# Performance work log

Hardware: AMD Instinct MI355X
Metric: run time of the kernel (lower is better)

## Reference

```python
import jax, jax.numpy as jnp
import numpy as np

# Matches init_kwargs: zip(dilation_rates, sequence_lengths)
DILATION_RATES = (1, 2, 4)
SEQUENCE_LENGTHS = (2048, 4096, 8192)


def setup_inputs() -> dict:
    key = jax.random.key(0)
    qkv = jax.random.normal(key, (4, 8192, 3, 16, 64), dtype=jnp.float32)
    return {"qkv": qkv}


def _attend(x, scale):
    # x: (B', Nseg, 3, h, d) -- vanilla softmax attention over axis Nseg
    q, k, v = x[:, :, 0], x[:, :, 1], x[:, :, 2]
    scores = jnp.einsum('bnhd,bmhd->bhnm', q, k) * scale
    attn = jax.nn.softmax(scores, axis=-1)
    return jnp.einsum('bhnm,bmhd->bnhd', attn, v)  # (B', Nseg, h, d)


def reference(qkv):
    b, n, _, h, d = qkv.shape
    scale = 1.0 / jnp.sqrt(jnp.asarray(d, qkv.dtype))  # softmax_scale=None default
    out = jnp.zeros((b, n, h, d), qkv.dtype)
    for r, s in zip(DILATION_RATES, SEQUENCE_LENGTHS):
        nseg = n // s
        # 'b (n s) qkv h d -> b n s qkv h d' then dilated slice [::r]
        x = qkv.reshape(b, nseg, s, 3, h, d)[:, :, ::r]  # (b, nseg, sp, 3, h, d)
        sp = x.shape[2]
        # 'b n s qkv h d -> (b s) n qkv h d'
        x = x.transpose(0, 2, 1, 3, 4, 5).reshape(b * sp, nseg, 3, h, d)
        o = _attend(x, scale)  # (b*sp, nseg, h, d)
        # '(b s) n h d -> b n s h d'
        o = o.reshape(b, sp, nseg, h, d).transpose(0, 2, 1, 3, 4)
        # strided scatter-add back into the full-length accumulator
        out = out.reshape(b, nseg, s, h, d).at[:, :, ::r].add(o).reshape(b, n, h, d)
    # final global normalization over the sequence dim (as in the source)
    return out / out.sum(axis=1, keepdims=True)
```

## Files before the change

kernel.cpp:

```cpp
#include <hip/hip_runtime.h>

constexpr int   Bn    = 4;
constexpr int   Nn    = 8192;
constexpr int   Hn    = 16;
constexpr int   Dn    = 64;
constexpr int   ROW   = 3 * Hn * Dn;
constexpr long long QKV_B = (long long)Nn * ROW;
constexpr int   OUT_N = Hn * Dn;
constexpr long long OUT_B = (long long)Nn * OUT_N;
constexpr long long OUT_TOT = (long long)Bn * OUT_B;
constexpr int   NBLK  = 2048;
constexpr int   BLKS_PER_B = 512;

using v4f = __attribute__((ext_vector_type(4))) float;
using v4u = __attribute__((ext_vector_type(4))) unsigned int;

template<int CTRL>
__device__ __forceinline__ float dpp_add(float x) {
  int mv = __builtin_amdgcn_update_dpp(0, __float_as_int(x), CTRL, 0xF, 0xF, true);
  return x + __int_as_float(mv);
}
__device__ __forceinline__ float row16_sum(float x) {
  x = dpp_add<0xB1>(x);
  x = dpp_add<0x4E>(x);
  x = dpp_add<0x124>(x);
  x = dpp_add<0x128>(x);
  return x;
}

__device__ __forceinline__ unsigned short f2bf_rne(float x) {
  unsigned u = __float_as_uint(x);
  u += 0x7FFFu + ((u >> 16) & 1u);
  return (unsigned short)(u >> 16);
}

struct Frag {
  float q[4][4], k[4][4], v[4][4];
};

__device__ __forceinline__ void load_frag(Frag& f, const float* __restrict__ qb,
                                          int j) {
#pragma unroll
  for (int m = 0; m < 4; ++m) {
    const float* rp = qb + (size_t)(m * 2048 + j) * ROW;
    float4 t;
    t = *(const float4*)(rp);
    f.q[m][0] = t.x; f.q[m][1] = t.y; f.q[m][2] = t.z; f.q[m][3] = t.w;
    t = *(const float4*)(rp + 1024);
    f.k[m][0] = t.x; f.k[m][1] = t.y; f.k[m][2] = t.z; f.k[m][3] = t.w;
    t = *(const float4*)(rp + 2048);
    f.v[m][0] = t.x; f.v[m][1] = t.y; f.v[m][2] = t.z; f.v[m][3] = t.w;
  }
}

template<bool USE_BF16>
__device__ __forceinline__ void compute_frag(const Frag& f, int j, size_t obase,
                                             float* __restrict__ out,
                                             unsigned short* __restrict__ ws16,
                                             float* cs) {
  float S[4][4];
#pragma unroll
  for (int m = 0; m < 4; ++m)
#pragma unroll
    for (int m2 = 0; m2 < 4; ++m2) {
      float s = f.q[m][0] * f.k[m2][0] + f.q[m][1] * f.k[m2][1] +
                f.q[m][2] * f.k[m2][2] + f.q[m][3] * f.k[m2][3];
      S[m][m2] = row16_sum(s) * 0.125f;
    }

  float acc[4][4];

#pragma unroll
  for (int m = 0; m < 4; ++m) {
    float mx = fmaxf(fmaxf(S[m][0], S[m][1]), fmaxf(S[m][2], S[m][3]));
    float e0 = __expf(S[m][0] - mx);
    float e1 = __expf(S[m][1] - mx);
    float e2 = __expf(S[m][2] - mx);
    float e3 = __expf(S[m][3] - mx);
    float inv = 1.0f / (e0 + e1 + e2 + e3);
    e0 *= inv; e1 *= inv; e2 *= inv; e3 *= inv;
#pragma unroll
    for (int c = 0; c < 4; ++c)
      acc[m][c] = e0 * f.v[0][c] + e1 * f.v[1][c] +
                  e2 * f.v[2][c] + e3 * f.v[3][c];
  }

  if ((j & 1) == 0) {
#pragma unroll
    for (int m = 0; m < 4; ++m) {
      const int a  = m & 1;
      const int b2 = a + 2;
      float sa = S[m][a], sb = S[m][b2];
      float mx = fmaxf(sa, sb);
      float ea = __expf(sa - mx);
      float eb = __expf(sb - mx);
      float inv = 1.0f / (ea + eb);
      ea *= inv; eb *= inv;
#pragma unroll
      for (int c = 0; c < 4; ++c)
        acc[m][c] += ea * f.v[a][c] + eb * f.v[b2][c];
    }
  }

  if ((j & 3) == 0) {
#pragma unroll
    for (int m = 0; m < 4; ++m)
#pragma unroll
      for (int c = 0; c < 4; ++c)
        acc[m][c] += f.v[m][c];
  }

#pragma unroll
  for (int m = 0; m < 4; ++m) {
    const size_t oi = obase + (size_t)(m * 2048 + j) * OUT_N;
    if (USE_BF16) {
      ushort4 st;
      st.x = f2bf_rne(acc[m][0]); st.y = f2bf_rne(acc[m][1]);
      st.z = f2bf_rne(acc[m][2]); st.w = f2bf_rne(acc[m][3]);
      *(ushort4*)(ws16 + oi) = st;
    } else {
      *(float4*)(out + oi) =
          make_float4(acc[m][0], acc[m][1], acc[m][2], acc[m][3]);
    }
    cs[0] += acc[m][0]; cs[1] += acc[m][1];
    cs[2] += acc[m][2]; cs[3] += acc[m][3];
  }
}

template<bool USE_BF16>
__global__ __launch_bounds__(256) void dil_main(const float* __restrict__ qkv,
                                                float* __restrict__ out,
                                                unsigned short* __restrict__ ws16,
                                                float* __restrict__ partial) {
  const int tid  = threadIdx.x;
  const int bid  = blockIdx.x;
  const int b    = bid >> 9;
  const int j0   = (bid & 511) * 4;

  const float* qb = qkv + (size_t)b * QKV_B + tid * 4;
  const size_t obase = (size_t)b * OUT_B + tid * 4;

  float cs[4] = {0.f, 0.f, 0.f, 0.f};

  Frag A, B;
  load_frag(A, qb, j0);
  load_frag(B, qb, j0 + 1);
  __builtin_amdgcn_sched_barrier(0);
  compute_frag<USE_BF16>(A, j0, obase, out, ws16, cs);
  load_frag(A, qb, j0 + 2);
  __builtin_amdgcn_sched_barrier(0);
  compute_frag<USE_BF16>(B, j0 + 1, obase, out, ws16, cs);
  load_frag(B, qb, j0 + 3);
  __builtin_amdgcn_sched_barrier(0);
  compute_frag<USE_BF16>(A, j0 + 2, obase, out, ws16, cs);
  compute_frag<USE_BF16>(B, j0 + 3, obase, out, ws16, cs);

  *(float4*)(partial + (size_t)bid * 1024 + tid * 4) =
      make_float4(cs[0], cs[1], cs[2], cs[3]);
}

__global__ __launch_bounds__(256) void dil_recip(const float* __restrict__ partial,
                                                 float* __restrict__ recip) {
  const int i = blockIdx.x * 256 + threadIdx.x;
  const int b = i >> 10;
  const int w = i & 1023;
  const float* p = partial + (size_t)b * BLKS_PER_B * 1024 + w;
  double s0 = 0.0, s1 = 0.0, s2 = 0.0, s3 = 0.0;
  double s4 = 0.0, s5 = 0.0, s6 = 0.0, s7 = 0.0;
  for (int r = 0; r < BLKS_PER_B; r += 8) {
    float f0 = p[(size_t)(r + 0) * 1024];
    float f1 = p[(size_t)(r + 1) * 1024];
    float f2 = p[(size_t)(r + 2) * 1024];
    float f3 = p[(size_t)(r + 3) * 1024];
    float f4 = p[(size_t)(r + 4) * 1024];
    float f5 = p[(size_t)(r + 5) * 1024];
    float f6 = p[(size_t)(r + 6) * 1024];
    float f7 = p[(size_t)(r + 7) * 1024];
    s0 += (double)f0; s1 += (double)f1; s2 += (double)f2; s3 += (double)f3;
    s4 += (double)f4; s5 += (double)f5; s6 += (double)f6; s7 += (double)f7;
  }
  double s = ((s0 + s1) + (s2 + s3)) + ((s4 + s5) + (s6 + s7));
  recip[i] = (float)(1.0 / s);
}

__global__ __launch_bounds__(256) void dil_scale_bf16(const unsigned short* __restrict__ ws16,
                                                      float* __restrict__ out,
                                                      const float* __restrict__ recip) {
  const long long u = (long long)blockIdx.x * 256 + threadIdx.x;
  const long long e = u * 8;
  const int b  = (int)(e >> 23);
  const int h  = (int)((e >> 6) & 15);
  const int q8 = (int)((e >> 3) & 7);

  const float4 r0 = ((const float4*)recip)[((b * 16 + h) << 4) + q8 * 2];
  const float4 r1 = ((const float4*)recip)[((b * 16 + h) << 4) + q8 * 2 + 1];

  const uint4 raw = *(const uint4*)(ws16 + e);
  v4f o0, o1;
  o0[0] = __uint_as_float((raw.x & 0xFFFFu) << 16) * r0.x;
  o0[1] = __uint_as_float((raw.x & 0xFFFF0000u))   * r0.y;
  o0[2] = __uint_as_float((raw.y & 0xFFFFu) << 16) * r0.z;
  o0[3] = __uint_as_float((raw.y & 0xFFFF0000u))   * r0.w;
  o1[0] = __uint_as_float((raw.z & 0xFFFFu) << 16) * r1.x;
  o1[1] = __uint_as_float((raw.z & 0xFFFF0000u))   * r1.y;
  o1[2] = __uint_as_float((raw.w & 0xFFFFu) << 16) * r1.z;
  o1[3] = __uint_as_float((raw.w & 0xFFFF0000u))   * r1.w;
  __builtin_nontemporal_store(o0, (v4f*)(out + e));
  __builtin_nontemporal_store(o1, (v4f*)(out + e + 4));
}

__global__ __launch_bounds__(256) void dil_scale_f32(float* __restrict__ out,
                                                     const float* __restrict__ recip) {
  const long long f = (long long)blockIdx.x * 256 + threadIdx.x;
  const int d4 = (int)(f & 15);
  const int h  = (int)((f >> 4) & 15);
  const int b  = (int)(f >> 21);
  const float4 r = ((const float4*)recip)[(b * 16 + h) * 16 + d4];
  float4 o = ((const float4*)out)[f];
  o.x *= r.x; o.y *= r.y; o.z *= r.z; o.w *= r.w;
  ((float4*)out)[f] = o;
}

extern "C" void kernel_launch(void* const* d_in, const int* in_sizes, int n_in,
                              void* d_out, int out_size, void* d_ws, size_t ws_size,
                              hipStream_t stream) {
  const float* qkv = (const float*)d_in[0];
  float* out = (float*)d_out;

  const size_t bf16_bytes    = (size_t)OUT_TOT * 2;
  const size_t partial_bytes = (size_t)NBLK * 1024 * 4;
  const size_t recip_bytes   = 4096 * sizeof(float);

  bool use_bf16 = (bf16_bytes + partial_bytes + recip_bytes) <= ws_size;

  unsigned short* ws16 = (unsigned short*)d_ws;
  char* tail = (char*)d_ws + (use_bf16 ? bf16_bytes : 0);
  float* partial = (float*)tail;
  float* recip   = (float*)(tail + partial_bytes);

  if (use_bf16)
    dil_main<true><<<NBLK, 256, 0, stream>>>(qkv, out, ws16, partial);
  else
    dil_main<false><<<NBLK, 256, 0, stream>>>(qkv, out, ws16, partial);

  dil_recip<<<16, 256, 0, stream>>>(partial, recip);

  if (use_bf16) {
    const long long nu = OUT_TOT / 8;
    dil_scale_bf16<<<(int)(nu / 256), 256, 0, stream>>>(ws16, out, recip);
  } else {
    const long long nf4 = OUT_TOT / 4;
    dil_scale_f32<<<(int)(nf4 / 256), 256, 0, stream>>>(out, recip);
  }
}
```

Measured before the change: 150.3 us.

## Remap threads to 8-element slices with two teams per block

Each thread now handles 8 contiguous head-dim elements instead of 4, so a head's dot product reduces across 8 lanes with three DPP steps instead of 16 lanes with four. The block is split into two 128-thread teams that each process two sequence positions, and their column partial sums are combined through shared memory before the per-block partial is written. This drops the explicit software double-buffered prefetch in favour of more independent loads per thread. It raises register pressure and adds a block-wide barrier plus LDS traffic for the partial-sum merge.

```diff
diff --git a/kernel.cpp b/kernel.cpp
--- a/kernel.cpp
+++ b/kernel.cpp
@@ -12,19 +12,18 @@
 constexpr int   NBLK  = 2048;
 constexpr int   BLKS_PER_B = 512;
 
-using v4f = __attribute__((ext_vector_type(4))) float;
-using v4u = __attribute__((ext_vector_type(4))) unsigned int;
+using v4f   = __attribute__((ext_vector_type(4))) float;
+using u16x8 = __attribute__((ext_vector_type(8))) unsigned short;
 
 template<int CTRL>
 __device__ __forceinline__ float dpp_add(float x) {
   int mv = __builtin_amdgcn_update_dpp(0, __float_as_int(x), CTRL, 0xF, 0xF, true);
   return x + __int_as_float(mv);
 }
-__device__ __forceinline__ float row16_sum(float x) {
+__device__ __forceinline__ float row8_sum(float x) {
   x = dpp_add<0xB1>(x);
   x = dpp_add<0x4E>(x);
-  x = dpp_add<0x124>(x);
-  x = dpp_add<0x128>(x);
+  x = dpp_add<0x141>(x);
   return x;
 }
 
@@ -32,99 +31,6 @@
   unsigned u = __float_as_uint(x);
   u += 0x7FFFu + ((u >> 16) & 1u);
   return (unsigned short)(u >> 16);
-}
-
-struct Frag {
-  float q[4][4], k[4][4], v[4][4];
-};
-
-__device__ __forceinline__ void load_frag(Frag& f, const float* __restrict__ qb,
-                                          int j) {
-#pragma unroll
-  for (int m = 0; m < 4; ++m) {
-    const float* rp = qb + (size_t)(m * 2048 + j) * ROW;
-    float4 t;
-    t = *(const float4*)(rp);
-    f.q[m][0] = t.x; f.q[m][1] = t.y; f.q[m][2] = t.z; f.q[m][3] = t.w;
-    t = *(const float4*)(rp + 1024);
-    f.k[m][0] = t.x; f.k[m][1] = t.y; f.k[m][2] = t.z; f.k[m][3] = t.w;
-    t = *(const float4*)(rp + 2048);
-    f.v[m][0] = t.x; f.v[m][1] = t.y; f.v[m][2] = t.z; f.v[m][3] = t.w;
-  }
-}
-
-template<bool USE_BF16>
-__device__ __forceinline__ void compute_frag(const Frag& f, int j, size_t obase,
-                                             float* __restrict__ out,
-                                             unsigned short* __restrict__ ws16,
-                                             float* cs) {
-  float S[4][4];
-#pragma unroll
-  for (int m = 0; m < 4; ++m)
-#pragma unroll
-    for (int m2 = 0; m2 < 4; ++m2) {
-      float s = f.q[m][0] * f.k[m2][0] + f.q[m][1] * f.k[m2][1] +
-                f.q[m][2] * f.k[m2][2] + f.q[m][3] * f.k[m2][3];
-      S[m][m2] = row16_sum(s) * 0.125f;
-    }
-
-  float acc[4][4];
-
-#pragma unroll
-  for (int m = 0; m < 4; ++m) {
-    float mx = fmaxf(fmaxf(S[m][0], S[m][1]), fmaxf(S[m][2], S[m][3]));
-    float e0 = __expf(S[m][0] - mx);
-    float e1 = __expf(S[m][1] - mx);
-    float e2 = __expf(S[m][2] - mx);
-    float e3 = __expf(S[m][3] - mx);
-    float inv = 1.0f / (e0 + e1 + e2 + e3);
-    e0 *= inv; e1 *= inv; e2 *= inv; e3 *= inv;
-#pragma unroll
-    for (int c = 0; c < 4; ++c)
-      acc[m][c] = e0 * f.v[0][c] + e1 * f.v[1][c] +
-                  e2 * f.v[2][c] + e3 * f.v[3][c];
-  }
-
-  if ((j & 1) == 0) {
-#pragma unroll
-    for (int m = 0; m < 4; ++m) {
-      const int a  = m & 1;
-      const int b2 = a + 2;
-      float sa = S[m][a], sb = S[m][b2];
-      float mx = fmaxf(sa, sb);
-      float ea = __expf(sa - mx);
-      float eb = __expf(sb - mx);
-      float inv = 1.0f / (ea + eb);
-      ea *= inv; eb *= inv;
-#pragma unroll
-      for (int c = 0; c < 4; ++c)
-        acc[m][c] += ea * f.v[a][c] + eb * f.v[b2][c];
-    }
-  }
-
-  if ((j & 3) == 0) {
-#pragma unroll
-    for (int m = 0; m < 4; ++m)
-#pragma unroll
-      for (int c = 0; c < 4; ++c)
-        acc[m][c] += f.v[m][c];
-  }
-
-#pragma unroll
-  for (int m = 0; m < 4; ++m) {
-    const size_t oi = obase + (size_t)(m * 2048 + j) * OUT_N;
-    if (USE_BF16) {
-      ushort4 st;
-      st.x = f2bf_rne(acc[m][0]); st.y = f2bf_rne(acc[m][1]);
-      st.z = f2bf_rne(acc[m][2]); st.w = f2bf_rne(acc[m][3]);
-      *(ushort4*)(ws16 + oi) = st;
-    } else {
-      *(float4*)(out + oi) =
-          make_float4(acc[m][0], acc[m][1], acc[m][2], acc[m][3]);
-    }
-    cs[0] += acc[m][0]; cs[1] += acc[m][1];
-    cs[2] += acc[m][2]; cs[3] += acc[m][3];
-  }
 }
 
 template<bool USE_BF16>
@@ -132,31 +38,125 @@
                                                 float* __restrict__ out,
                                                 unsigned short* __restrict__ ws16,
                                                 float* __restrict__ partial) {
+  __shared__ float xrow[1024];
   const int tid  = threadIdx.x;
+  const int team = tid >> 7;
+  const int lt   = tid & 127;
+  const int off  = lt * 8;
   const int bid  = blockIdx.x;
   const int b    = bid >> 9;
-  const int j0   = (bid & 511) * 4;
-
-  const float* qb = qkv + (size_t)b * QKV_B + tid * 4;
-  const size_t obase = (size_t)b * OUT_B + tid * 4;
-
-  float cs[4] = {0.f, 0.f, 0.f, 0.f};
-
-  Frag A, B;
-  load_frag(A, qb, j0);
-  load_frag(B, qb, j0 + 1);
-  __builtin_amdgcn_sched_barrier(0);
-  compute_frag<USE_BF16>(A, j0, obase, out, ws16, cs);
-  load_frag(A, qb, j0 + 2);
-  __builtin_amdgcn_sched_barrier(0);
-  compute_frag<USE_BF16>(B, j0 + 1, obase, out, ws16, cs);
-  load_frag(B, qb, j0 + 3);
-  __builtin_amdgcn_sched_barrier(0);
-  compute_frag<USE_BF16>(A, j0 + 2, obase, out, ws16, cs);
-  compute_frag<USE_BF16>(B, j0 + 3, obase, out, ws16, cs);
-
-  *(float4*)(partial + (size_t)bid * 1024 + tid * 4) =
-      make_float4(cs[0], cs[1], cs[2], cs[3]);
+  const int jc   = bid & 511;
+
+  const float* qb = qkv + (size_t)b * QKV_B + off;
+  const size_t obase = (size_t)b * OUT_B + off;
+
+  float cs[8] = {0.f, 0.f, 0.f, 0.f, 0.f, 0.f, 0.f, 0.f};
+
+#pragma unroll
+  for (int it = 0; it < 2; ++it) {
+    const int j = jc * 4 + it * 2 + team;
+
+    float q[4][8], k[4][8], v[4][8];
+#pragma unroll
+    for (int m = 0; m < 4; ++m) {
+      const float* rp = qb + (size_t)(m * 2048 + j) * ROW;
+      *(float4*)&q[m][0] = *(const float4*)(rp);
+      *(float4*)&q[m][4] = *(const float4*)(rp + 4);
+      *(float4*)&k[m][0] = *(const float4*)(rp + 1024);
+      *(float4*)&k[m][4] = *(const float4*)(rp + 1028);
+      *(float4*)&v[m][0] = *(const float4*)(rp + 2048);
+      *(float4*)&v[m][4] = *(const float4*)(rp + 2052);
+    }
+
+    float S[4][4];
+#pragma unroll
+    for (int m = 0; m < 4; ++m)
+#pragma unroll
+      for (int m2 = 0; m2 < 4; ++m2) {
+        float s = 0.f;
+#pragma unroll
+        for (int c = 0; c < 8; ++c)
+          s += q[m][c] * k[m2][c];
+        S[m][m2] = row8_sum(s) * 0.125f;
+      }
+
+    float acc[4][8];
+
+#pragma unroll
+    for (int m = 0; m < 4; ++m) {
+      float mx = fmaxf(fmaxf(S[m][0], S[m][1]), fmaxf(S[m][2], S[m][3]));
+      float e0 = __expf(S[m][0] - mx);
+      float e1 = __expf(S[m][1] - mx);
+      float e2 = __expf(S[m][2] - mx);
+      float e3 = __expf(S[m][3] - mx);
+      float inv = 1.0f / (e0 + e1 + e2 + e3);
+      e0 *= inv; e1 *= inv; e2 *= inv; e3 *= inv;
+#pragma unroll
+      for (int c = 0; c < 8; ++c)
+        acc[m][c] = e0 * v[0][c] + e1 * v[1][c] + e2 * v[2][c] + e3 * v[3][c];
+    }
+
+    if ((j & 1) == 0) {
+#pragma unroll
+      for (int m = 0; m < 4; ++m) {
+        const int a  = m & 1;
+        const int b2 = a + 2;
+        float sa = S[m][a], sb = S[m][b2];
+        float mx = fmaxf(sa, sb);
+        float ea = __expf(sa - mx);
+        float eb = __expf(sb - mx);
+        float inv = 1.0f / (ea + eb);
+        ea *= inv; eb *= inv;
+#pragma unroll
+        for (int c = 0; c < 8; ++c)
+          acc[m][c] += ea * v[a][c] + eb * v[b2][c];
+      }
+    }
+
+    if ((j & 3) == 0) {
+#pragma unroll
+      for (int m = 0; m < 4; ++m)
+#pragma unroll
+        for (int c = 0; c < 8; ++c)
+          acc[m][c] += v[m][c];
+    }
+
+#pragma unroll
+    for (int m = 0; m < 4; ++m) {
+      const size_t oi = obase + (size_t)(m * 2048 + j) * OUT_N;
+      if (USE_BF16) {
+        u16x8 st;
+#pragma unroll
+        for (int c = 0; c < 8; ++c)
+          st[c] = f2bf_rne(acc[m][c]);
+        *(u16x8*)(ws16 + oi) = st;
+      } else {
+        *(float4*)(out + oi) =
+            make_float4(acc[m][0], acc[m][1], acc[m][2], acc[m][3]);
+        *(float4*)(out + oi + 4) =
+            make_float4(acc[m][4], acc[m][5], acc[m][6], acc[m][7]);
+      }
+#pragma unroll
+      for (int c = 0; c < 8; ++c)
+        cs[c] += acc[m][c];
+    }
+  }
+
+  if (team == 1) {
+    *(float4*)&xrow[off]     = make_float4(cs[0], cs[1], cs[2], cs[3]);
+    *(float4*)&xrow[off + 4] = make_float4(cs[4], cs[5], cs[6], cs[7]);
+  }
+  __syncthreads();
+  if (team == 0) {
+    const float4 a = *(const float4*)&xrow[off];
+    const float4 bb = *(const float4*)&xrow[off + 4];
+    cs[0] += a.x;  cs[1] += a.y;  cs[2] += a.z;  cs[3] += a.w;
+    cs[4] += bb.x; cs[5] += bb.y; cs[6] += bb.z; cs[7] += bb.w;
+    *(float4*)(partial + (size_t)bid * 1024 + off) =
+        make_float4(cs[0], cs[1], cs[2], cs[3]);
+    *(float4*)(partial + (size_t)bid * 1024 + off + 4) =
+        make_float4(cs[4], cs[5], cs[6], cs[7]);
+  }
 }
 
 __global__ __launch_bounds__(256) void dil_recip(const float* __restrict__ partial,
```

After: 154.5 us. 2.8% more time.
